# Kernel optimization log

Measured on AMD Instinct MI355X. Metric: run time of the kernel, lower is better.

Reference implementation:

```python
import jax, jax.numpy as jnp
import numpy as np

B = 512      # number of agents (batch)
H = 64       # hidden_size
E = 64       # embadding_size
HP = 64      # relative-position embedding size in social pooling
OBS = 8      # observed track length
PRE = 12     # predict_length (pre_frame)


def setup_inputs() -> dict:
    key = jax.random.key(0)
    ks = jax.random.split(key, 10)
    def rn(k, shape, s=0.1):
        return jax.random.normal(k, shape, dtype=jnp.float32) * s
    return {
        "hidden_state": rn(ks[0], (1, B, H), 1.0),   # social hidden state from encoder
        "group_track": rn(ks[1], (B, OBS, 2), 1.0),  # ragged tracks regularized to OBS steps
        "W_emb": rn(ks[2], (2, E)),  "b_emb": jnp.zeros((E,), jnp.float32),
        "W_ih": rn(ks[3], (3 * H, E)), "W_hh": rn(ks[4], (3 * H, H)),
        "b_ih": jnp.zeros((3 * H,), jnp.float32), "b_hh": jnp.zeros((3 * H,), jnp.float32),
        "W_pos": rn(ks[5], (H, 2)), "b_pos": jnp.zeros((2,), jnp.float32),
        "W_rel": rn(ks[6], (2, HP)), "b_rel": jnp.zeros((HP,), jnp.float32),
        "W_pool": rn(ks[7], (HP + H, H)), "b_pool": jnp.zeros((H,), jnp.float32),
    }


def _gru_step(x, h, W_ih, W_hh, b_ih, b_hh):
    # torch nn.GRU single-layer step. x:[B,E], h:[B,H]
    gi = x @ W_ih.T + b_ih  # [B,3H]
    gh = h @ W_hh.T + b_hh
    i_r, i_z, i_n = jnp.split(gi, 3, axis=-1)
    h_r, h_z, h_n = jnp.split(gh, 3, axis=-1)
    r = jax.nn.sigmoid(i_r + h_r)
    z = jax.nn.sigmoid(i_z + h_z)
    n = jnp.tanh(i_n + r * h_n)
    return (1.0 - z) * n + z * h


def _spool(h, last_pos, W_rel, b_rel, W_pool, b_pool):
    # SGAN-style social pooling: embed pairwise relative last positions,
    # concat with each neighbor's hidden state, MLP, max-pool over neighbors.
    # h:[B,H], last_pos:[B,2] -> pooled:[B,H]
    rel = last_pos[None, :, :] - last_pos[:, None, :]          # [B,B,2]
    e = jax.nn.relu(rel @ W_rel + b_rel)                       # [B,B,HP]
    hj = jnp.broadcast_to(h[None, :, :], (h.shape[0], h.shape[0], h.shape[1]))
    feat = jnp.concatenate([e, hj], axis=-1)                   # [B,B,HP+H]
    m = jax.nn.relu(feat @ W_pool + b_pool)                    # [B,B,H]
    return jnp.max(m, axis=1)                                  # [B,H]


def reference(hidden_state, group_track, W_emb, b_emb, W_ih, W_hh, b_ih, b_hh,
              W_pos, b_pos, W_rel, b_rel, W_pool, b_pool):
    # Step 0: pool on encoder hidden state, GRU starts from zero state
    last = group_track[:, -1, :]                               # [B,2]
    pooled = _spool(hidden_state[0], last, W_rel, b_rel, W_pool, b_pool)
    pos0 = pooled @ W_pos + b_pos                              # [B,2]
    emb0 = pos0 @ W_emb + b_emb                                # [B,E]
    h0 = jnp.zeros((B, H), dtype=hidden_state.dtype)
    h = _gru_step(emb0, h0, W_ih, W_hh, b_ih, b_hh)

    def step(carry, _):
        h, last = carry
        pooled = _spool(h, last, W_rel, b_rel, W_pool, b_pool)  # pooling_p_step == 1
        pos = pooled @ W_pos + b_pos                            # [B,2]
        emb = pos @ W_emb + b_emb
        h_new = _gru_step(emb, h, W_ih, W_hh, b_ih, b_hh)
        return (h_new, pos), pos

    (_, _), poses = jax.lax.scan(step, (h, pos0), None, length=PRE - 1)  # [PRE-1,B,2]
    all_pos = jnp.concatenate([pos0[None], poses], axis=0)               # [PRE,B,2]
    # group_track grows by one position per step -> [B, OBS+PRE, 2]
    return jnp.concatenate([group_track, jnp.transpose(all_pos, (1, 0, 2))], axis=1)
```

## Files before the change

### kernel.cpp

```cpp
#include <hip/hip_runtime.h>
#include <math.h>

#define NB   512
#define NH   64
#define OBS  8
#define PRE  12

#define OFF_WREL  0
#define OFF_BREL  128
#define OFF_BPOOL 192
#define OFF_WPOS  256
#define OFF_BPOS  384
#define OFF_WEMB  386
#define OFF_BEMB  514
#define OFF_BIH   578
#define OFF_BHH   770
#define OFF_FLAG  962
#define N_SMALL   963

#define WS_BAR    0
#define WS_SMALL  4096
#define WS_WTF    8192
#define WS_WPBF   106496
#define WS_LAST   122880
#define WS_HBF    229376
#define WS_TOTAL  1134592
#define LAST_STRIDE_F2  1024
#define HBF_STRIDE_U16  34816

typedef __bf16 bf16x8 __attribute__((ext_vector_type(8)));
typedef float  f32x4  __attribute__((ext_vector_type(4)));

union FragU { bf16x8 v; unsigned short u[8]; };

__device__ __forceinline__ float bf2f(unsigned short u) {
  unsigned int x = ((unsigned int)u) << 16;
  return __builtin_bit_cast(float, x);
}
__device__ __forceinline__ unsigned short f2bf(float f) {
  unsigned int u = __builtin_bit_cast(unsigned int, f);
  u += 0x7FFFu + ((u >> 16) & 1u);
  return (unsigned short)(u >> 16);
}
__device__ __forceinline__ float ldf(const void* p, int i, bool isf32) {
  return isf32 ? ((const float*)p)[i] : bf2f(((const unsigned short*)p)[i]);
}
__device__ __forceinline__ unsigned short ld16(const void* p, int i, bool isf32) {
  return isf32 ? f2bf(((const float*)p)[i]) : ((const unsigned short*)p)[i];
}
__device__ __forceinline__ void stout(void* p, int i, float v, bool isf32) {
  if (isf32) ((float*)p)[i] = v;
  else       ((unsigned short*)p)[i] = f2bf(v);
}

__device__ __forceinline__ void st32_sc(unsigned* p, unsigned v) {
  __hip_atomic_store(p, v, __ATOMIC_RELAXED, __HIP_MEMORY_SCOPE_AGENT);
}
__device__ __forceinline__ void stf_sc(float* p, float v) {
  __hip_atomic_store(p, v, __ATOMIC_RELAXED, __HIP_MEMORY_SCOPE_AGENT);
}
__device__ __forceinline__ void st64_sc(void* p, unsigned long long v) {
  __hip_atomic_store((unsigned long long*)p, v, __ATOMIC_RELAXED, __HIP_MEMORY_SCOPE_AGENT);
}

__device__ __forceinline__ void grid_barrier(unsigned* bar, unsigned phase,
                                             int tid, int bid) {
  __syncthreads();
  if (tid == 0) {
    asm volatile("s_waitcnt vmcnt(0)" ::: "memory");
    unsigned prev = __hip_atomic_fetch_add(&bar[bid & 31], 1u,
                                           __ATOMIC_RELAXED, __HIP_MEMORY_SCOPE_AGENT);
    if ((prev & 15u) == 15u) {
      unsigned r = __hip_atomic_fetch_add(&bar[64], 1u,
                                          __ATOMIC_RELAXED, __HIP_MEMORY_SCOPE_AGENT);
      if ((r & 31u) == 31u) {
        __hip_atomic_store(&bar[96], (r >> 5) + 1u,
                           __ATOMIC_RELAXED, __HIP_MEMORY_SCOPE_AGENT);
      }
    }
    while (__hip_atomic_load(&bar[96], __ATOMIC_RELAXED,
                             __HIP_MEMORY_SCOPE_AGENT) < phase)
      __builtin_amdgcn_s_sleep(2);
  }
  __syncthreads();
}

__global__ __launch_bounds__(128) void init_kernel(unsigned* bar) {
  bar[threadIdx.x] = 0;
}

__global__ __launch_bounds__(256, 2) void fused_kernel(
    const void* __restrict__ hidden_state,
    const void* __restrict__ group_track,
    const void* __restrict__ W_emb,  const void* __restrict__ b_emb,
    const void* __restrict__ W_ih,   const void* __restrict__ W_hh,
    const void* __restrict__ b_ih,   const void* __restrict__ b_hh,
    const void* __restrict__ W_pos,  const void* __restrict__ b_pos,
    const void* __restrict__ W_rel,  const void* __restrict__ b_rel,
    const void* __restrict__ W_pool, const void* __restrict__ b_pool,
    float2* __restrict__ lastbase,
    unsigned short* __restrict__ hbfbase,
    float* __restrict__ WTf,
    unsigned short* __restrict__ Wp_bf,
    float* __restrict__ smallf,
    unsigned* __restrict__ bar,
    void* __restrict__ out)
{
  const int i    = blockIdx.x;
  const int tid  = threadIdx.x;
  const int lane = tid & 63;
  const int wave = tid >> 6;
  const int col  = lane & 15;
  const int quad = lane >> 4;

  __shared__ float  red[4][64];
  __shared__ float  part[4][6][64];
  __shared__ float  hstate[64];
  __shared__ float2 lpos[512];

  int bad = 0;
  const unsigned short* hs16 = (const unsigned short*)hidden_state;
  for (int k = lane; k < 256; k += 64) {
    unsigned e = (hs16[k] >> 7) & 0xFFu;
    bad |= (e >= 0x8Eu) ? 1 : 0;
  }
  const bool isf32 = (__ballot(bad) != 0ULL);

  if (tid < 32) {
    unsigned lo = ld16(hidden_state, i * 64 + 2 * tid,     isf32);
    unsigned hi = ld16(hidden_state, i * 64 + 2 * tid + 1, isf32);
    st32_sc((unsigned*)hbfbase + i * 32 + tid, lo | (hi << 16));
  }
  if (tid < 64) hstate[tid] = 0.0f;
  if (tid < 16) stout(out, i * 40 + tid, ldf(group_track, i * 16 + tid, isf32), isf32);
  if (tid == 0) {
    float2 l0;
    l0.x = ldf(group_track, i * 16 + 14, isf32);
    l0.y = ldf(group_track, i * 16 + 15, isf32);
    st64_sc(lastbase + i, __builtin_bit_cast(unsigned long long, l0));
  }

  if (i < 96) {
    int u = i * 256 + tid;
    int k = u / 384, c = u % 384;
    float v = (c < 192) ? ldf(W_ih, c * 64 + k, isf32)
                        : ldf(W_hh, (c - 192) * 64 + k, isf32);
    stf_sc(&WTf[u], v);
  } else if (i < 112) {
    int u = (i - 96) * 256 + tid;
    unsigned lo = ld16(W_pool, 2 * u,     isf32);
    unsigned hi = ld16(W_pool, 2 * u + 1, isf32);
    st32_sc((unsigned*)Wp_bf + u, lo | (hi << 16));
  } else if (i >= 128 && i < 132) {
    int u = (i - 128) * 256 + tid;
    if (u < N_SMALL) {
      float v;
      if      (u < 128) v = ldf(W_rel,  u,        isf32);
      else if (u < 192) v = ldf(b_rel,  u - 128,  isf32);
      else if (u < 256) v = ldf(b_pool, u - 192,  isf32);
      else if (u < 384) v = ldf(W_pos,  u - 256,  isf32);
      else if (u < 386) v = ldf(b_pos,  u - 384,  isf32);
      else if (u < 514) v = ldf(W_emb,  u - 386,  isf32);
      else if (u < 578) v = ldf(b_emb,  u - 514,  isf32);
      else if (u < 770) v = ldf(b_ih,   u - 578,  isf32);
      else if (u < 962) v = ldf(b_hh,   u - 770,  isf32);
      else              v = isf32 ? 1.0f : 0.0f;
      stf_sc(&smallf[u], v);
    }
  }
  grid_barrier(bar, 1u, tid, i);

  float wr0[2][8], wr1[2][8], brl[2][8];
  #pragma unroll
  for (int ks = 0; ks < 2; ++ks) {
    int kb = ks * 32 + quad * 8;
    #pragma unroll
    for (int j = 0; j < 8; ++j) {
      wr0[ks][j] = smallf[OFF_WREL + kb + j];
      wr1[ks][j] = smallf[OFF_WREL + 64 + kb + j];
      brl[ks][j] = smallf[OFF_BREL + kb + j];
    }
  }
  float bp[4];
  #pragma unroll
  for (int nt = 0; nt < 4; ++nt) bp[nt] = smallf[OFF_BPOOL + nt * 16 + col];

  FragU bw[4][4];
  #pragma unroll
  for (int nt = 0; nt < 4; ++nt)
    #pragma unroll
    for (int ks = 0; ks < 4; ++ks)
      #pragma unroll
      for (int j = 0; j < 8; ++j)
        bw[nt][ks].u[j] = Wp_bf[(ks * 32 + quad * 8 + j) * 64 + nt * 16 + col];

  for (int t = 0; t < PRE; ++t) {
    const float2*         lp       = lastbase + t * LAST_STRIDE_F2;
    float2*               last_out = lastbase + (t + 1) * LAST_STRIDE_F2;
    const unsigned short* hbf_in   = hbfbase + t * HBF_STRIDE_U16;
    unsigned short*       hbf_out  = hbfbase + (t + 1) * HBF_STRIDE_U16;

    lpos[tid]       = lp[tid];
    lpos[tid + 256] = lp[tid + 256];
    __syncthreads();
    const float2 li = lpos[i];

    float vmax[4] = {0.f, 0.f, 0.f, 0.f};

    const int jb0 = wave * 128;
    for (int s = 0; s < 4; ++s) {
      const int jb = jb0 + s * 32;
      const int r0 = jb + col, r1 = r0 + 16;
      const float2 l0 = lpos[r0], l1 = lpos[r1];
      const float d0x = l0.x - li.x, d0y = l0.y - li.y;
      const float d1x = l1.x - li.x, d1y = l1.y - li.y;

      FragU aE[2][2];
      #pragma unroll
      for (int ks = 0; ks < 2; ++ks) {
        #pragma unroll
        for (int j = 0; j < 8; ++j) {
          float e0 = fmaxf(d0x * wr0[ks][j] + d0y * wr1[ks][j] + brl[ks][j], 0.f);
          float e1 = fmaxf(d1x * wr0[ks][j] + d1y * wr1[ks][j] + brl[ks][j], 0.f);
          aE[0][ks].u[j] = f2bf(e0);
          aE[1][ks].u[j] = f2bf(e1);
        }
      }
      bf16x8 aH[2][2];
      #pragma unroll
      for (int mt = 0; mt < 2; ++mt) {
        int jr = jb + mt * 16 + col;
        #pragma unroll
        for (int ks = 0; ks < 2; ++ks)
          aH[mt][ks] = *(const bf16x8*)(hbf_in + jr * 64 + ks * 32 + quad * 8);
      }

      f32x4 acc[2][4];
      #pragma unroll
      for (int mt = 0; mt < 2; ++mt)
        #pragma unroll
        for (int nt = 0; nt < 4; ++nt)
          acc[mt][nt] = (f32x4){0.f, 0.f, 0.f, 0.f};

      #pragma unroll
      for (int nt = 0; nt < 4; ++nt)
        #pragma unroll
        for (int mt = 0; mt < 2; ++mt) {
          acc[mt][nt] = __builtin_amdgcn_mfma_f32_16x16x32_bf16(aE[mt][0].v, bw[nt][0].v, acc[mt][nt], 0, 0, 0);
          acc[mt][nt] = __builtin_amdgcn_mfma_f32_16x16x32_bf16(aE[mt][1].v, bw[nt][1].v, acc[mt][nt], 0, 0, 0);
          acc[mt][nt] = __builtin_amdgcn_mfma_f32_16x16x32_bf16(aH[mt][0],   bw[nt][2].v, acc[mt][nt], 0, 0, 0);
          acc[mt][nt] = __builtin_amdgcn_mfma_f32_16x16x32_bf16(aH[mt][1],   bw[nt][3].v, acc[mt][nt], 0, 0, 0);
        }

      #pragma unroll
      for (int mt = 0; mt < 2; ++mt)
        #pragma unroll
        for (int nt = 0; nt < 4; ++nt)
          #pragma unroll
          for (int r = 0; r < 4; ++r) {
            float v = acc[mt][nt][r] + bp[nt];
            vmax[nt] = fmaxf(fmaxf(v, 0.f), vmax[nt]);
          }
    }

    #pragma unroll
    for (int nt = 0; nt < 4; ++nt) {
      vmax[nt] = fmaxf(vmax[nt], __shfl_xor(vmax[nt], 16, 64));
      vmax[nt] = fmaxf(vmax[nt], __shfl_xor(vmax[nt], 32, 64));
    }
    if (lane < 16) {
      #pragma unroll
      for (int nt = 0; nt < 4; ++nt) red[wave][nt * 16 + lane] = vmax[nt];
    }
    __syncthreads();

    {
      const int o = lane;
      float pooled = fmaxf(fmaxf(red[0][o], red[1][o]), fmaxf(red[2][o], red[3][o]));
      float p0 = pooled * smallf[OFF_WPOS + o * 2 + 0];
      float p1 = pooled * smallf[OFF_WPOS + o * 2 + 1];
      #pragma unroll
      for (int sft = 32; sft >= 1; sft >>= 1) {
        p0 += __shfl_xor(p0, sft, 64);
        p1 += __shfl_xor(p1, sft, 64);
      }
      p0 += smallf[OFF_BPOS + 0];
      p1 += smallf[OFF_BPOS + 1];

      float g0 = 0.f, g1 = 0.f, g2 = 0.f, g3 = 0.f, g4 = 0.f, g5 = 0.f;
      #pragma unroll 8
      for (int kk = 0; kk < 16; ++kk) {
        int k = wave * 16 + kk;
        float ek = p0 * smallf[OFF_WEMB + k] + p1 * smallf[OFF_WEMB + 64 + k]
                 + smallf[OFF_BEMB + k];
        float hk = hstate[k];
        const float* w = WTf + k * 384;
        g0 += ek * w[o];
        g1 += ek * w[64 + o];
        g2 += ek * w[128 + o];
        g3 += hk * w[192 + o];
        g4 += hk * w[256 + o];
        g5 += hk * w[320 + o];
      }
      part[wave][0][o] = g0; part[wave][1][o] = g1; part[wave][2][o] = g2;
      part[wave][3][o] = g3; part[wave][4][o] = g4; part[wave][5][o] = g5;
      __syncthreads();

      if (wave == 0) {
        float gir = 0.f, giz = 0.f, gin = 0.f, ghr = 0.f, ghz = 0.f, ghn = 0.f;
        #pragma unroll
        for (int pp = 0; pp < 4; ++pp) {
          gir += part[pp][0][o]; giz += part[pp][1][o]; gin += part[pp][2][o];
          ghr += part[pp][3][o]; ghz += part[pp][4][o]; ghn += part[pp][5][o];
        }
        gir += smallf[OFF_BIH + o];       ghr += smallf[OFF_BHH + o];
        giz += smallf[OFF_BIH + 64 + o];  ghz += smallf[OFF_BHH + 64 + o];
        gin += smallf[OFF_BIH + 128 + o]; ghn += smallf[OFF_BHH + 128 + o];
        float r = 1.f / (1.f + __expf(-(gir + ghr)));
        float z = 1.f / (1.f + __expf(-(giz + ghz)));
        float n = tanhf(gin + r * ghn);
        float hp = hstate[o];
        float hn = (1.f - z) * n + z * hp;
        hstate[o] = hn;
        int hbi = (int)f2bf(hn);
        unsigned v0 = (unsigned)__shfl(hbi, (o & 31) * 2, 64);
        unsigned v1 = (unsigned)__shfl(hbi, (o & 31) * 2 + 1, 64);
        if (o < 32)
          st32_sc((unsigned*)hbf_out + i * 32 + o, v0 | (v1 << 16));
        if (o == 0) {
          stout(out, i * 40 + (OBS + t) * 2 + 0, p0, isf32);
          stout(out, i * 40 + (OBS + t) * 2 + 1, p1, isf32);
          float2 pr; pr.x = p0; pr.y = p1;
          st64_sc(last_out + i, __builtin_bit_cast(unsigned long long, pr));
        }
      }
    }

    if (t < PRE - 1) grid_barrier(bar, (unsigned)(t + 2), tid, i);
  }
}

__global__ __launch_bounds__(64) void prep_kernel(
    const void* __restrict__ hidden_state,
    const void* __restrict__ group_track,
    const void* __restrict__ W_emb,  const void* __restrict__ b_emb,
    const void* __restrict__ W_ih,   const void* __restrict__ W_hh,
    const void* __restrict__ b_ih,   const void* __restrict__ b_hh,
    const void* __restrict__ W_pos,  const void* __restrict__ b_pos,
    const void* __restrict__ W_rel,  const void* __restrict__ b_rel,
    const void* __restrict__ W_pool, const void* __restrict__ b_pool,
    float* __restrict__ last0,
    unsigned short* __restrict__ hbf0,
    float* __restrict__ h_carry,
    float* __restrict__ WTf,
    unsigned short* __restrict__ Wp_bf,
    float* __restrict__ smallf,
    void* __restrict__ out)
{
  const int b = blockIdx.x;
  const int o = threadIdx.x;

  int bad = 0;
  const unsigned short* hs16 = (const unsigned short*)hidden_state;
  for (int k = o; k < 256; k += 64) {
    unsigned e = (hs16[k] >> 7) & 0xFFu;
    bad |= (e >= 0x8Eu) ? 1 : 0;
  }
  const bool isf32 = (__ballot(bad) != 0ULL);

  hbf0[b * 64 + o] = ld16(hidden_state, b * 64 + o, isf32);
  h_carry[b * 64 + o] = 0.0f;
  if (o < 16) stout(out, b * 40 + o, ldf(group_track, b * 16 + o, isf32), isf32);
  if (o < 2)  last0[b * 2 + o] = ldf(group_track, b * 16 + 14 + o, isf32);

  if (b < 384) {
    int u = b * 64 + o;
    int k = u / 384, c = u % 384;
    WTf[u] = (c < 192) ? ldf(W_ih, c * 64 + k, isf32)
                       : ldf(W_hh, (c - 192) * 64 + k, isf32);
  } else {
    int u = (b - 384) * 64 + o;
    Wp_bf[u] = ld16(W_pool, u, isf32);
  }

  if (b < 16) {
    int u = b * 64 + o;
    if (u < N_SMALL) {
      float v;
      if      (u < 128) v = ldf(W_rel,  u,        isf32);
      else if (u < 192) v = ldf(b_rel,  u - 128,  isf32);
      else if (u < 256) v = ldf(b_pool, u - 192,  isf32);
      else if (u < 384) v = ldf(W_pos,  u - 256,  isf32);
      else if (u < 386) v = ldf(b_pos,  u - 384,  isf32);
      else if (u < 514) v = ldf(W_emb,  u - 386,  isf32);
      else if (u < 578) v = ldf(b_emb,  u - 514,  isf32);
      else if (u < 770) v = ldf(b_ih,   u - 578,  isf32);
      else if (u < 962) v = ldf(b_hh,   u - 770,  isf32);
      else              v = isf32 ? 1.0f : 0.0f;
      smallf[u] = v;
    }
  }
}

__global__ __launch_bounds__(256) void pair_kernel(
    const float* __restrict__ smallf,
    const unsigned short* __restrict__ Wp_bf,
    const float* __restrict__ WTf,
    const float* __restrict__ last_in,
    float* __restrict__ last_out,
    const unsigned short* __restrict__ hbf_in,
    unsigned short* __restrict__ hbf_out,
    float* __restrict__ h_carry,
    void* __restrict__ out,
    int t)
{
  const int i    = blockIdx.x;
  const int tid  = threadIdx.x;
  const int lane = tid & 63;
  const int wave = tid >> 6;
  const int col  = lane & 15;
  const int quad = lane >> 4;

  __shared__ float red[4][64];

  const float2* lp = (const float2*)last_in;
  const float2  li = lp[i];

  float wr0[2][8], wr1[2][8], brl[2][8];
  #pragma unroll
  for (int ks = 0; ks < 2; ++ks) {
    int kb = ks * 32 + quad * 8;
    #pragma unroll
    for (int j = 0; j < 8; ++j) {
      wr0[ks][j] = smallf[OFF_WREL + kb + j];
      wr1[ks][j] = smallf[OFF_WREL + 64 + kb + j];
      brl[ks][j] = smallf[OFF_BREL + kb + j];
    }
  }
  float bp[4];
  #pragma unroll
  for (int nt = 0; nt < 4; ++nt) bp[nt] = smallf[OFF_BPOOL + nt * 16 + col];

  FragU bw[4][4];
  #pragma unroll
  for (int nt = 0; nt < 4; ++nt)
    #pragma unroll
    for (int ks = 0; ks < 4; ++ks)
      #pragma unroll
      for (int j = 0; j < 8; ++j)
        bw[nt][ks].u[j] = Wp_bf[(ks * 32 + quad * 8 + j) * 64 + nt * 16 + col];

  float vmax[4] = {0.f, 0.f, 0.f, 0.f};

  const int jb0 = wave * 128;
  for (int s = 0; s < 4; ++s) {
    const int jb = jb0 + s * 32;
    const int r0 = jb + col, r1 = r0 + 16;
    const float2 l0 = lp[r0], l1 = lp[r1];
    const float d0x = l0.x - li.x, d0y = l0.y - li.y;
    const float d1x = l1.x - li.x, d1y = l1.y - li.y;

    FragU aE[2][2];
    #pragma unroll
    for (int ks = 0; ks < 2; ++ks) {
      #pragma unroll
      for (int j = 0; j < 8; ++j) {
        float e0 = fmaxf(d0x * wr0[ks][j] + d0y * wr1[ks][j] + brl[ks][j], 0.f);
        float e1 = fmaxf(d1x * wr0[ks][j] + d1y * wr1[ks][j] + brl[ks][j], 0.f);
        aE[0][ks].u[j] = f2bf(e0);
        aE[1][ks].u[j] = f2bf(e1);
      }
    }
    bf16x8 aH[2][2];
    #pragma unroll
    for (int mt = 0; mt < 2; ++mt) {
      int jr = jb + mt * 16 + col;
      #pragma unroll
      for (int ks = 0; ks < 2; ++ks)
        aH[mt][ks] = *(const bf16x8*)(hbf_in + jr * 64 + ks * 32 + quad * 8);
    }

    f32x4 acc[2][4];
    #pragma unroll
    for (int mt = 0; mt < 2; ++mt)
      #pragma unroll
      for (int nt = 0; nt < 4; ++nt)
        acc[mt][nt] = (f32x4){0.f, 0.f, 0.f, 0.f};

    #pragma unroll
    for (int nt = 0; nt < 4; ++nt)
      #pragma unroll
      for (int mt = 0; mt < 2; ++mt) {
        acc[mt][nt] = __builtin_amdgcn_mfma_f32_16x16x32_bf16(aE[mt][0].v, bw[nt][0].v, acc[mt][nt], 0, 0, 0);
        acc[mt][nt] = __builtin_amdgcn_mfma_f32_16x16x32_bf16(aE[mt][1].v, bw[nt][1].v, acc[mt][nt], 0, 0, 0);
        acc[mt][nt] = __builtin_amdgcn_mfma_f32_16x16x32_bf16(aH[mt][0],   bw[nt][2].v, acc[mt][nt], 0, 0, 0);
        acc[mt][nt] = __builtin_amdgcn_mfma_f32_16x16x32_bf16(aH[mt][1],   bw[nt][3].v, acc[mt][nt], 0, 0, 0);
      }

    #pragma unroll
    for (int mt = 0; mt < 2; ++mt)
      #pragma unroll
      for (int nt = 0; nt < 4; ++nt)
        #pragma unroll
        for (int r = 0; r < 4; ++r) {
          float v = acc[mt][nt][r] + bp[nt];
          vmax[nt] = fmaxf(fmaxf(v, 0.f), vmax[nt]);
        }
  }

  #pragma unroll
  for (int nt = 0; nt < 4; ++nt) {
    vmax[nt] = fmaxf(vmax[nt], __shfl_xor(vmax[nt], 16, 64));
    vmax[nt] = fmaxf(vmax[nt], __shfl_xor(vmax[nt], 32, 64));
  }
  if (lane < 16) {
    #pragma unroll
    for (int nt = 0; nt < 4; ++nt) red[wave][nt * 16 + lane] = vmax[nt];
  }
  __syncthreads();

  if (tid < 64) {
    const int o = tid;
    const bool isf32 = (smallf[OFF_FLAG] != 0.0f);
    float pooled = fmaxf(fmaxf(red[0][o], red[1][o]), fmaxf(red[2][o], red[3][o]));
    float p0 = pooled * smallf[OFF_WPOS + o * 2 + 0];
    float p1 = pooled * smallf[OFF_WPOS + o * 2 + 1];
    #pragma unroll
    for (int sft = 32; sft >= 1; sft >>= 1) {
      p0 += __shfl_xor(p0, sft, 64);
      p1 += __shfl_xor(p1, sft, 64);
    }
    p0 += smallf[OFF_BPOS + 0];
    p1 += smallf[OFF_BPOS + 1];
    if (o == 0) {
      stout(out, i * 40 + (OBS + t) * 2 + 0, p0, isf32);
      stout(out, i * 40 + (OBS + t) * 2 + 1, p1, isf32);
      last_out[2 * i]     = p0;
      last_out[2 * i + 1] = p1;
    }
    float gir = 0.f, giz = 0.f, gin = 0.f, ghr = 0.f, ghz = 0.f, ghn = 0.f;
    #pragma unroll 8
    for (int k = 0; k < 64; ++k) {
      float ek = p0 * smallf[OFF_WEMB + k] + p1 * smallf[OFF_WEMB + 64 + k]
               + smallf[OFF_BEMB + k];
      float hk = h_carry[i * 64 + k];
      const float* w = WTf + k * 384;
      gir += ek * w[o];
      giz += ek * w[64 + o];
      gin += ek * w[128 + o];
      ghr += hk * w[192 + o];
      ghz += hk * w[256 + o];
      ghn += hk * w[320 + o];
    }
    gir += smallf[OFF_BIH + o];       ghr += smallf[OFF_BHH + o];
    giz += smallf[OFF_BIH + 64 + o];  ghz += smallf[OFF_BHH + 64 + o];
    gin += smallf[OFF_BIH + 128 + o]; ghn += smallf[OFF_BHH + 128 + o];
    float r = 1.f / (1.f + __expf(-(gir + ghr)));
    float z = 1.f / (1.f + __expf(-(giz + ghz)));
    float n = tanhf(gin + r * ghn);
    float hp = h_carry[i * 64 + o];
    float hn = (1.f - z) * n + z * hp;
    h_carry[i * 64 + o] = hn;
    hbf_out[i * 64 + o] = f2bf(hn);
  }
}

extern "C" void kernel_launch(void* const* d_in, const int* in_sizes, int n_in,
                              void* d_out, int out_size, void* d_ws, size_t ws_size,
                              hipStream_t stream) {
  (void)in_sizes; (void)n_in; (void)out_size;
  const void* hidden_state = d_in[0];
  const void* group_track  = d_in[1];
  const void* W_emb  = d_in[2];
  const void* b_emb  = d_in[3];
  const void* W_ih   = d_in[4];
  const void* W_hh   = d_in[5];
  const void* b_ih   = d_in[6];
  const void* b_hh   = d_in[7];
  const void* W_pos  = d_in[8];
  const void* b_pos  = d_in[9];
  const void* W_rel  = d_in[10];
  const void* b_rel  = d_in[11];
  const void* W_pool = d_in[12];
  const void* b_pool = d_in[13];

  char* ws = (char*)d_ws;

  if (ws_size >= WS_TOTAL) {
    unsigned*       bar      = (unsigned*)(ws + WS_BAR);
    float*          smallf   = (float*)(ws + WS_SMALL);
    float*          WTf      = (float*)(ws + WS_WTF);
    unsigned short* Wp_bf    = (unsigned short*)(ws + WS_WPBF);
    float2*         lastbase = (float2*)(ws + WS_LAST);
    unsigned short* hbfbase  = (unsigned short*)(ws + WS_HBF);

    init_kernel<<<1, 128, 0, stream>>>(bar);
    fused_kernel<<<NB, 256, 0, stream>>>(hidden_state, group_track,
                                         W_emb, b_emb, W_ih, W_hh, b_ih, b_hh,
                                         W_pos, b_pos, W_rel, b_rel,
                                         W_pool, b_pool,
                                         lastbase, hbfbase,
                                         WTf, Wp_bf, smallf, bar, d_out);
    return;
  }

  float* lastA            = (float*)(ws + 0);
  float* lastB            = (float*)(ws + 4096);
  unsigned short* hbfA    = (unsigned short*)(ws + 8192);
  unsigned short* hbfB    = (unsigned short*)(ws + 73728);
  float* h_carry          = (float*)(ws + 139264);
  float* WTf              = (float*)(ws + 270336);
  unsigned short* Wp_bf   = (unsigned short*)(ws + 368640);
  float* smallf           = (float*)(ws + 385024);

  prep_kernel<<<512, 64, 0, stream>>>(hidden_state, group_track,
                                      W_emb, b_emb, W_ih, W_hh, b_ih, b_hh,
                                      W_pos, b_pos, W_rel, b_rel, W_pool, b_pool,
                                      lastA, hbfA, h_carry, WTf, Wp_bf,
                                      smallf, d_out);
  float* lastBuf[2] = {lastA, lastB};
  unsigned short* hbfBuf[2] = {hbfA, hbfB};
  for (int t = 0; t < PRE; ++t) {
    int p = t & 1;
    pair_kernel<<<512, 256, 0, stream>>>(smallf, Wp_bf, WTf,
                                         lastBuf[p], lastBuf[1 - p],
                                         hbfBuf[p], hbfBuf[1 - p],
                                         h_carry, d_out, t);
  }
}
```

Baseline: 237.6 us.

## Drop LDS staging of positions and trim per-step barrier and pooling overhead

Each step used to copy all 512 last positions into shared memory and then run a block sync. That staging is removed: neighbor positions are read directly from global memory, and each block's own position is carried in a register and updated from the computed output. Bias add and ReLU move out of the inner max loop, applied once after the running max. The step-end grid barrier drops its leading __syncthreads, and the spin-wait sleep is lengthened. The aim is to cut per-step latency in this barrier-bound recurrence. The risks are more global loads per tile, a missing intra-block ordering step, and slower wake-up from the longer sleep.

```diff
diff --git a/kernel.cpp b/kernel.cpp
--- a/kernel.cpp
+++ b/kernel.cpp
@@ -63,9 +63,8 @@
   __hip_atomic_store((unsigned long long*)p, v, __ATOMIC_RELAXED, __HIP_MEMORY_SCOPE_AGENT);
 }
 
-__device__ __forceinline__ void grid_barrier(unsigned* bar, unsigned phase,
-                                             int tid, int bid) {
-  __syncthreads();
+__device__ __forceinline__ void grid_barrier_core(unsigned* bar, unsigned phase,
+                                                  int tid, int bid) {
   if (tid == 0) {
     asm volatile("s_waitcnt vmcnt(0)" ::: "memory");
     unsigned prev = __hip_atomic_fetch_add(&bar[bid & 31], 1u,
@@ -80,9 +79,14 @@
     }
     while (__hip_atomic_load(&bar[96], __ATOMIC_RELAXED,
                              __HIP_MEMORY_SCOPE_AGENT) < phase)
-      __builtin_amdgcn_s_sleep(2);
+      __builtin_amdgcn_s_sleep(8);
   }
   __syncthreads();
+}
+__device__ __forceinline__ void grid_barrier_full(unsigned* bar, unsigned phase,
+                                                  int tid, int bid) {
+  __syncthreads();
+  grid_barrier_core(bar, phase, tid, bid);
 }
 
 __global__ __launch_bounds__(128) void init_kernel(unsigned* bar) {
@@ -113,10 +117,9 @@
   const int col  = lane & 15;
   const int quad = lane >> 4;
 
-  __shared__ float  red[4][64];
-  __shared__ float  part[4][6][64];
-  __shared__ float  hstate[64];
-  __shared__ float2 lpos[512];
+  __shared__ float red[4][64];
+  __shared__ float part[4][6][64];
+  __shared__ float hstate[64];
 
   int bad = 0;
   const unsigned short* hs16 = (const unsigned short*)hidden_state;
@@ -133,12 +136,11 @@
   }
   if (tid < 64) hstate[tid] = 0.0f;
   if (tid < 16) stout(out, i * 40 + tid, ldf(group_track, i * 16 + tid, isf32), isf32);
-  if (tid == 0) {
-    float2 l0;
-    l0.x = ldf(group_track, i * 16 + 14, isf32);
-    l0.y = ldf(group_track, i * 16 + 15, isf32);
-    st64_sc(lastbase + i, __builtin_bit_cast(unsigned long long, l0));
-  }
+  float2 li;
+  li.x = ldf(group_track, i * 16 + 14, isf32);
+  li.y = ldf(group_track, i * 16 + 15, isf32);
+  if (tid == 0)
+    st64_sc(lastbase + i, __builtin_bit_cast(unsigned long long, li));
 
   if (i < 96) {
     int u = i * 256 + tid;
@@ -168,7 +170,7 @@
       stf_sc(&smallf[u], v);
     }
   }
-  grid_barrier(bar, 1u, tid, i);
+  grid_barrier_full(bar, 1u, tid, i);
 
   float wr0[2][8], wr1[2][8], brl[2][8];
   #pragma unroll
@@ -200,30 +202,25 @@
     const unsigned short* hbf_in   = hbfbase + t * HBF_STRIDE_U16;
     unsigned short*       hbf_out  = hbfbase + (t + 1) * HBF_STRIDE_U16;
 
-    lpos[tid]       = lp[tid];
-    lpos[tid + 256] = lp[tid + 256];
-    __syncthreads();
-    const float2 li = lpos[i];
-
-    float vmax[4] = {0.f, 0.f, 0.f, 0.f};
+    float mx[4] = {-3.0e38f, -3.0e38f, -3.0e38f, -3.0e38f};
 
     const int jb0 = wave * 128;
     for (int s = 0; s < 4; ++s) {
       const int jb = jb0 + s * 32;
       const int r0 = jb + col, r1 = r0 + 16;
-      const float2 l0 = lpos[r0], l1 = lpos[r1];
+      const float2 l0 = lp[r0], l1 = lp[r1];
       const float d0x = l0.x - li.x, d0y = l0.y - li.y;
       const float d1x = l1.x - li.x, d1y = l1.y - li.y;
 
-      FragU aE[2][2];
+      bf16x8 aE[2][2];
       #pragma unroll
       for (int ks = 0; ks < 2; ++ks) {
         #pragma unroll
         for (int j = 0; j < 8; ++j) {
           float e0 = fmaxf(d0x * wr0[ks][j] + d0y * wr1[ks][j] + brl[ks][j], 0.f);
           float e1 = fmaxf(d1x * wr0[ks][j] + d1y * wr1[ks][j] + brl[ks][j], 0.f);
-          aE[0][ks].u[j] = f2bf(e0);
-          aE[1][ks].u[j] = f2bf(e1);
+          aE[0][ks][j] = (__bf16)e0;
+          aE[1][ks][j] = (__bf16)e1;
         }
       }
       bf16x8 aH[2][2];
@@ -246,25 +243,26 @@
       for (int nt = 0; nt < 4; ++nt)
         #pragma unroll
         for (int mt = 0; mt < 2; ++mt) {
-          acc[mt][nt] = __builtin_amdgcn_mfma_f32_16x16x32_bf16(aE[mt][0].v, bw[nt][0].v, acc[mt][nt], 0, 0, 0);
-          acc[mt][nt] = __builtin_amdgcn_mfma_f32_16x16x32_bf16(aE[mt][1].v, bw[nt][1].v, acc[mt][nt], 0, 0, 0);
-          acc[mt][nt] = __builtin_amdgcn_mfma_f32_16x16x32_bf16(aH[mt][0],   bw[nt][2].v, acc[mt][nt], 0, 0, 0);
-          acc[mt][nt] = __builtin_amdgcn_mfma_f32_16x16x32_bf16(aH[mt][1],   bw[nt][3].v, acc[mt][nt], 0, 0, 0);
+          acc[mt][nt] = __builtin_amdgcn_mfma_f32_16x16x32_bf16(aE[mt][0], bw[nt][0].v, acc[mt][nt], 0, 0, 0);
+          acc[mt][nt] = __builtin_amdgcn_mfma_f32_16x16x32_bf16(aE[mt][1], bw[nt][1].v, acc[mt][nt], 0, 0, 0);
+          acc[mt][nt] = __builtin_amdgcn_mfma_f32_16x16x32_bf16(aH[mt][0], bw[nt][2].v, acc[mt][nt], 0, 0, 0);
+          acc[mt][nt] = __builtin_amdgcn_mfma_f32_16x16x32_bf16(aH[mt][1], bw[nt][3].v, acc[mt][nt], 0, 0, 0);
         }
 
       #pragma unroll
       for (int mt = 0; mt < 2; ++mt)
         #pragma unroll
-        for (int nt = 0; nt < 4; ++nt)
-          #pragma unroll
-          for (int r = 0; r < 4; ++r) {
-            float v = acc[mt][nt][r] + bp[nt];
-            vmax[nt] = fmaxf(fmaxf(v, 0.f), vmax[nt]);
-          }
-    }
-
+        for (int nt = 0; nt < 4; ++nt) {
+          float m01 = fmaxf(acc[mt][nt][0], acc[mt][nt][1]);
+          float m23 = fmaxf(acc[mt][nt][2], acc[mt][nt][3]);
+          mx[nt] = fmaxf(fmaxf(m01, m23), mx[nt]);
+        }
+    }
+
+    float vmax[4];
     #pragma unroll
     for (int nt = 0; nt < 4; ++nt) {
+      vmax[nt] = fmaxf(mx[nt] + bp[nt], 0.f);
       vmax[nt] = fmaxf(vmax[nt], __shfl_xor(vmax[nt], 16, 64));
       vmax[nt] = fmaxf(vmax[nt], __shfl_xor(vmax[nt], 32, 64));
     }
@@ -334,9 +332,11 @@
           st64_sc(last_out + i, __builtin_bit_cast(unsigned long long, pr));
         }
       }
-    }
-
-    if (t < PRE - 1) grid_barrier(bar, (unsigned)(t + 2), tid, i);
+      li.x = p0;
+      li.y = p1;
+    }
+
+    if (t < PRE - 1) grid_barrier_core(bar, (unsigned)(t + 2), tid, i);
   }
 }
 
```

Result: no change. 235.2 us (-1.0%).
